# Performance work log

Measured on AMD Instinct MI355X. Metric: run time of the kernel, lower is better.

## Reference

```python
import jax, jax.numpy as jnp
import numpy as np

N = 100000   # nodes
F = 32       # input features
E = 1600000  # edges
G = 512      # graphs
EPS = 1e-5   # BatchNorm eps


def setup_inputs() -> dict:
    key = jax.random.key(0)
    ks = jax.random.split(key, 12)
    x = jax.random.normal(ks[0], (N, F), jnp.float32)
    edge_index = jax.random.randint(ks[1], (2, E), 0, N)
    batch = jnp.sort(jax.random.randint(ks[2], (N,), 0, G))

    def glorot(k, i, o):
        return jax.random.normal(k, (i, o), jnp.float32) * (1.0 / np.sqrt(i))

    return {
        "x": x, "edge_index": edge_index, "batch": batch,
        "W1": glorot(ks[3], F, 16), "b1": jnp.zeros((16,), jnp.float32),
        "g1": jnp.ones((16,), jnp.float32), "be1": jnp.zeros((16,), jnp.float32),
        "W2": glorot(ks[4], 16, 64), "b2": jnp.zeros((64,), jnp.float32),
        "g2": jnp.ones((64,), jnp.float32), "be2": jnp.zeros((64,), jnp.float32),
        "W3": glorot(ks[5], 64, 64), "b3": jnp.zeros((64,), jnp.float32),
        "Wc": glorot(ks[6], 64, 1), "bc": jnp.zeros((1,), jnp.float32),
    }


def _gcn_conv(h, src, dst, dis, W, b, n):
    # PyG GCNConv: D^{-1/2}(A+I)D^{-1/2} X W + b (self-loops folded in analytically)
    hw = h @ W                                   # [N, out]
    msg = hw[src] * (dis[src] * dis[dst])[:, None]   # gather + normalize, [E, out]
    agg = jax.ops.segment_sum(msg, dst, num_segments=n)  # scatter-add
    agg = agg + hw * (dis * dis)[:, None]        # self-loop contribution
    return agg + b


def _bn(h, g, b):
    # BatchNorm1d, training mode (biased variance over node axis)
    m = jnp.mean(h, axis=0)
    v = jnp.mean((h - m) ** 2, axis=0)
    return (h - m) * jax.lax.rsqrt(v + EPS) * g + b


def reference(x, edge_index, batch, W1, b1, g1, be1, W2, b2, g2, be2, W3, b3, Wc, bc):
    n = x.shape[0]
    src, dst = edge_index[0], edge_index[1]
    # degree including self-loops (computed on target nodes, edge weight 1)
    deg = jax.ops.segment_sum(jnp.ones((src.shape[0],), x.dtype), dst, num_segments=n) + 1.0
    dis = jax.lax.rsqrt(deg)

    h = jnp.tanh(_gcn_conv(x, src, dst, dis, W1, b1, n))
    h = _bn(h, g1, be1)
    h = jnp.tanh(_gcn_conv(h, src, dst, dis, W2, b2, n))
    h = _bn(h, g2, be2)
    h = jnp.tanh(_gcn_conv(h, src, dst, dis, W3, b3, n))

    # global_mean_pool over graph ids
    sums = jax.ops.segment_sum(h, batch, num_segments=G)          # [G, 64]
    cnts = jax.ops.segment_sum(jnp.ones((n,), x.dtype), batch, num_segments=G)
    pooled = sums / jnp.maximum(cnts, 1.0)[:, None]

    return pooled @ Wc + bc   # [G, 1]
```

## Files before the change

kernel.cpp:

```cpp
#include <hip/hip_runtime.h>

#define EPSV 1e-5f
#define EB 512
#define NPB 256
#define NBUK_MAX 512

typedef __attribute__((ext_vector_type(8))) short bf16x8;
typedef __attribute__((ext_vector_type(4))) float f32x4;
typedef unsigned short ushort_t;

__device__ inline unsigned f2bf(float f){
  unsigned u = __float_as_uint(f);
  u += 0x7fffu + ((u>>16)&1u);
  return u>>16;
}
#define BF_LO(u) __uint_as_float((u)<<16)
#define BF_HI(u) __uint_as_float((u)&0xffff0000u)

__global__ __launch_bounds__(256) void k_csr_count(const int* __restrict__ dst, int E, int chunk,
                                                   int nbuk, int* __restrict__ cnt){
  __shared__ int hist[NBUK_MAX];
  int t = threadIdx.x, b = blockIdx.x;
  for(int k=t; k<nbuk; k+=256) hist[k]=0;
  __syncthreads();
  int lo = b*chunk, hi = lo+chunk < E ? lo+chunk : E;
  for(int i=lo+t; i<hi; i+=256) atomicAdd(&hist[dst[i]>>8], 1);
  __syncthreads();
  for(int k=t; k<nbuk; k+=256) cnt[(size_t)k*EB + b] = hist[k];
}

__global__ __launch_bounds__(1024) void k_scan_local(const int* __restrict__ v_in, int L,
                                                     int* __restrict__ loc, int* __restrict__ blk){
  __shared__ int ps[1024];
  int t = threadIdx.x;
  int i = blockIdx.x*1024 + t;
  int v = (i < L) ? v_in[i] : 0;
  ps[t] = v;
  __syncthreads();
  for(int off=1; off<1024; off<<=1){
    int u = (t>=off) ? ps[t-off] : 0;
    __syncthreads();
    ps[t] += u;
    __syncthreads();
  }
  if(i < L) loc[i] = ps[t] - v;
  if(t == 1023) blk[blockIdx.x] = ps[t];
}

__global__ __launch_bounds__(1024) void k_scan_sums(int* __restrict__ blk, int nb,
                                                    int* __restrict__ totalOut){
  __shared__ int ps[1024];
  int t = threadIdx.x;
  int v = (t < nb) ? blk[t] : 0;
  ps[t] = v;
  __syncthreads();
  for(int off=1; off<1024; off<<=1){
    int u = (t>=off) ? ps[t-off] : 0;
    __syncthreads();
    ps[t] += u;
    __syncthreads();
  }
  if(t < nb) blk[t] = ps[t] - v;
  if(t == 1023) *totalOut = ps[t];
}

__global__ __launch_bounds__(256) void k_csr_scatter(const int* __restrict__ src,
                                                     const int* __restrict__ dst,
                                                     const int* __restrict__ loc,
                                                     const int* __restrict__ blk,
                                                     int E, int chunk, int nbuk,
                                                     unsigned* __restrict__ epk){
  __shared__ int cur[NBUK_MAX];
  int t = threadIdx.x, b = blockIdx.x;
  for(int k=t; k<nbuk; k+=256){
    int i = k*EB + b;
    cur[k] = loc[i] + blk[i>>10];
  }
  __syncthreads();
  int lo = b*chunk, hi = lo+chunk < E ? lo+chunk : E;
  for(int i=lo+t; i<hi; i+=256){
    int d = dst[i];
    int p = atomicAdd(&cur[d>>8], 1);
    epk[p] = ((unsigned)src[i]<<8) | (unsigned)(d & 255);
  }
}

__global__ __launch_bounds__(256) void k_csr_final(const unsigned* __restrict__ epk,
                                                   const int* __restrict__ loc,
                                                   const int* __restrict__ blk,
                                                   int nbuk, int N, int E,
                                                   int* __restrict__ rp, float* __restrict__ dis,
                                                   int* __restrict__ csr_src){
  __shared__ int hist[NPB], ps[NPB], cur[NPB];
  int t = threadIdx.x, k = blockIdx.x;
  int i0 = k*EB;
  int base = loc[i0] + blk[i0>>10];
  int next;
  if(k+1 < nbuk){ int i1 = (k+1)*EB; next = loc[i1] + blk[i1>>10]; }
  else next = E;
  int cntk = next - base;
  int node0 = k*NPB;
  hist[t] = 0;
  __syncthreads();
  for(int i=t; i<cntk; i+=256) atomicAdd(&hist[(int)(epk[base+i] & 255u)], 1);
  __syncthreads();
  int deg = hist[t];
  ps[t] = deg;
  __syncthreads();
  for(int off=1; off<256; off<<=1){
    int u = (t>=off) ? ps[t-off] : 0;
    __syncthreads();
    ps[t] += u;
    __syncthreads();
  }
  int lb = ps[t] - deg;
  int n = node0 + t;
  if(n < N){
    rp[n]  = base + lb;
    dis[n] = rsqrtf((float)deg + 1.0f);
  }
  cur[t] = base + lb;
  __syncthreads();
  for(int i=t; i<cntk; i+=256){
    unsigned e = epk[base+i];
    int p = atomicAdd(&cur[(int)(e & 255u)], 1);
    csr_src[p] = (int)(e >> 8);
  }
  if(k == nbuk-1 && t == 0) rp[N] = E;
}

__global__ __launch_bounds__(256) void k_gemm1(const float* __restrict__ x,
                                               const float* __restrict__ W,
                                               const float* __restrict__ dis,
                                               int N, ushort_t* __restrict__ P1){
  __shared__ __align__(16) float Ws[32*16];
  int t = threadIdx.x;
  for(int i=t; i<32*16; i+=256) Ws[i] = W[i];
  __syncthreads();
  int row = blockIdx.x*256 + t;
  if(row >= N) return;
  const float4* xr = (const float4*)(x + (size_t)row*32);
  float acc[16];
  #pragma unroll
  for(int j=0;j<16;j++) acc[j]=0.f;
  #pragma unroll
  for(int k4=0;k4<8;k4++){
    float4 v = xr[k4];
    float vv[4] = {v.x, v.y, v.z, v.w};
    #pragma unroll
    for(int kk=0;kk<4;kk++){
      float h = vv[kk];
      const float* wr = &Ws[(k4*4+kk)*16];
      #pragma unroll
      for(int j=0;j<16;j++) acc[j] += h*wr[j];
    }
  }
  float d = dis[row];
  unsigned q[8];
  #pragma unroll
  for(int j=0;j<8;j++)
    q[j] = f2bf(acc[2*j]*d) | (f2bf(acc[2*j+1]*d)<<16);
  uint4* o = (uint4*)(P1 + (size_t)row*16);
  o[0] = make_uint4(q[0],q[1],q[2],q[3]);
  o[1] = make_uint4(q[4],q[5],q[6],q[7]);
}

__global__ __launch_bounds__(256) void k_gather1(const int* __restrict__ rp,
    const int* __restrict__ csr_src,
    const float* __restrict__ dis, const ushort_t* __restrict__ P1,
    const float* __restrict__ bias, int N, ushort_t* __restrict__ Q1,
    float* __restrict__ sdis, float* __restrict__ partials){
  int t = threadIdx.x;
  int idx = blockIdx.x*256 + t;
  int n = idx >> 1, g = t & 1;
  float v[8];
  #pragma unroll
  for(int j=0;j<8;j++) v[j]=0.f;

  if(n < N){
    int beg = rp[n], end = rp[n+1];
    uint4 u = *(const uint4*)(P1 + (size_t)n*16 + g*8);
    float a0 = BF_LO(u.x), a1 = BF_HI(u.x), a2 = BF_LO(u.y), a3 = BF_HI(u.y);
    float a4 = BF_LO(u.z), a5 = BF_HI(u.z), a6 = BF_LO(u.w), a7 = BF_HI(u.w);
    float b0=0.f,b1=0.f,b2=0.f,b3=0.f,b4=0.f,b5=0.f,b6=0.f,b7=0.f;
    float sd = 0.f;
    int j = beg;
    for(; j+1 < end; j += 2){
      int s0 = csr_src[j], s1 = csr_src[j+1];
      uint4 u0 = *(const uint4*)(P1 + (size_t)s0*16 + g*8);
      uint4 u1 = *(const uint4*)(P1 + (size_t)s1*16 + g*8);
      if(g==0) sd += dis[s0] + dis[s1];
      a0 += BF_LO(u0.x); a1 += BF_HI(u0.x); a2 += BF_LO(u0.y); a3 += BF_HI(u0.y);
      a4 += BF_LO(u0.z); a5 += BF_HI(u0.z); a6 += BF_LO(u0.w); a7 += BF_HI(u0.w);
      b0 += BF_LO(u1.x); b1 += BF_HI(u1.x); b2 += BF_LO(u1.y); b3 += BF_HI(u1.y);
      b4 += BF_LO(u1.z); b5 += BF_HI(u1.z); b6 += BF_LO(u1.w); b7 += BF_HI(u1.w);
    }
    if(j < end){
      int s0 = csr_src[j];
      uint4 u0 = *(const uint4*)(P1 + (size_t)s0*16 + g*8);
      if(g==0) sd += dis[s0];
      a0 += BF_LO(u0.x); a1 += BF_HI(u0.x); a2 += BF_LO(u0.y); a3 += BF_HI(u0.y);
      a4 += BF_LO(u0.z); a5 += BF_HI(u0.z); a6 += BF_LO(u0.w); a7 += BF_HI(u0.w);
    }
    float d = dis[n];
    float4 bb0 = *(const float4*)(bias + g*8);
    float4 bb1 = *(const float4*)(bias + g*8 + 4);
    v[0] = tanhf((a0+b0)*d + bb0.x); v[1] = tanhf((a1+b1)*d + bb0.y);
    v[2] = tanhf((a2+b2)*d + bb0.z); v[3] = tanhf((a3+b3)*d + bb0.w);
    v[4] = tanhf((a4+b4)*d + bb1.x); v[5] = tanhf((a5+b5)*d + bb1.y);
    v[6] = tanhf((a6+b6)*d + bb1.z); v[7] = tanhf((a7+b7)*d + bb1.w);
    uint4 o;
    o.x = f2bf(v[0]*d) | (f2bf(v[1]*d)<<16);
    o.y = f2bf(v[2]*d) | (f2bf(v[3]*d)<<16);
    o.z = f2bf(v[4]*d) | (f2bf(v[5]*d)<<16);
    o.w = f2bf(v[6]*d) | (f2bf(v[7]*d)<<16);
    *(uint4*)(Q1 + (size_t)n*16 + g*8) = o;
    if(g==0) sdis[n] = sd;
  }

  int lane = t & 63, wid = t >> 6;
  __shared__ float redS[4][2][8], redQ[4][2][8];
  #pragma unroll
  for(int j=0;j<8;j++){
    float s = v[j], q = v[j]*v[j];
    #pragma unroll
    for(int off=32; off>=2; off>>=1){
      s += __shfl_down(s, off, 64);
      q += __shfl_down(q, off, 64);
    }
    if(lane < 2){ redS[wid][lane][j] = s; redQ[wid][lane][j] = q; }
  }
  __syncthreads();
  if(t < 16){
    int gg = t>>3, j = t&7;
    float S = redS[0][gg][j]+redS[1][gg][j]+redS[2][gg][j]+redS[3][gg][j];
    float Q = redQ[0][gg][j]+redQ[1][gg][j]+redQ[2][gg][j]+redQ[3][gg][j];
    partials[(size_t)blockIdx.x*32 + t]      = S;
    partials[(size_t)blockIdx.x*32 + 16 + t] = Q;
  }
}

template<int C>
__global__ __launch_bounds__(256) void k_bn_red(const float* __restrict__ partials, int nblk,
                                                float* __restrict__ red){
  constexpr int W = 2*C;
  constexpr int RPF = 256/W;
  int t = threadIdx.x;
  int c = t % W, r0 = t / W;
  float acc = 0.f;
  for(int r = blockIdx.x*RPF + r0; r < nblk; r += 64*RPF)
    acc += partials[(size_t)r*W + c];
  __shared__ float ls[256];
  ls[t] = acc;
  __syncthreads();
  if(t < W){
    float s = 0.f;
    #pragma unroll
    for(int k=0;k<RPF;k++) s += ls[k*W + t];
    red[blockIdx.x*W + t] = s;
  }
}

template<int C>
__global__ __launch_bounds__(256) void k_bn_finprep2(const float* __restrict__ red,
                           const float* __restrict__ gw, const float* __restrict__ be,
                           float invN, const float* __restrict__ W,
                           float* __restrict__ Wp, float* __restrict__ cp){
  __shared__ float s0[C], s1[C], scf[C], shf[C];
  int t = threadIdx.x;
  if(t < 2*C){
    float s = 0.f;
    for(int r=0;r<64;r++) s += red[r*2*C + t];
    if(t < C) s0[t] = s; else s1[t-C] = s;
  }
  __syncthreads();
  if(t < C){
    float m = s0[t]*invN;
    float var = fmaxf(s1[t]*invN - m*m, 0.f);
    float inv = rsqrtf(var + EPSV);
    float sc = gw[t]*inv;
    scf[t] = sc;
    shf[t] = be[t] - m*sc;
  }
  __syncthreads();
  for(int i=t; i<C*64; i+=256){
    int k = i >> 6;
    Wp[i] = scf[k]*W[i];
  }
  if(t < 64){
    float s = 0.f;
    for(int k=0;k<C;k++) s += shf[k]*W[k*64 + t];
    cp[t] = s;
  }
}

__global__ __launch_bounds__(256) void k_bn_finprep3(const float* __restrict__ red,
                           const float* __restrict__ gw, const float* __restrict__ be,
                           float invN, const float* __restrict__ W,
                           ushort_t* __restrict__ wf, float* __restrict__ cp){
  __shared__ float s0[64], s1[64], scf[64], shf[64];
  int t = threadIdx.x;
  if(t < 128){
    float s = 0.f;
    for(int r=0;r<64;r++) s += red[r*128 + t];
    if(t < 64) s0[t] = s; else s1[t-64] = s;
  }
  __syncthreads();
  if(t < 64){
    float m = s0[t]*invN;
    float var = fmaxf(s1[t]*invN - m*m, 0.f);
    float inv = rsqrtf(var + EPSV);
    float sc = gw[t]*inv;
    scf[t] = sc;
    shf[t] = be[t] - m*sc;
  }
  __syncthreads();
  int total = 4*2*64*8;
  for(int idx=t; idx<total; idx+=256){
    int e = idx & 7;
    int l = (idx>>3) & 63;
    int slot = idx>>9;
    int ct = slot>>1, half = slot&1;
    int k = (l>>4)*8 + e + half*32;
    int col = ct*16 + (l&15);
    wf[idx] = (ushort_t)f2bf(scf[k]*W[k*64 + col]);
  }
  if(t < 64){
    float s = 0.f;
    for(int k=0;k<64;k++) s += shf[k]*W[k*64 + t];
    cp[t] = s;
  }
}

__global__ __launch_bounds__(256) void k_l2fused(const int* __restrict__ rp,
    const int* __restrict__ csr_src, const float* __restrict__ dis,
    const float* __restrict__ sdis, const ushort_t* __restrict__ Q1,
    const float* __restrict__ Wp, const float* __restrict__ cp,
    const float* __restrict__ bias, int N, ushort_t* __restrict__ Q2,
    float* __restrict__ partials){
  __shared__ __align__(16) float Wl[16*64];
  __shared__ float cpl[64], bl[64];
  int t = threadIdx.x;
  for(int i=t; i<16*64; i+=256) Wl[i] = Wp[i];
  if(t < 64){ cpl[t] = cp[t]; bl[t] = bias[t]; }
  __syncthreads();

  int idx = blockIdx.x*256 + t;
  int n = idx >> 3, g = t & 7;
  int half = g & 1, eo = g >> 1;
  bool valid = (n < N);
  float M8[8];
  #pragma unroll
  for(int j=0;j<8;j++) M8[j]=0.f;

  if(valid){
    int beg = rp[n], end = rp[n+1];
    if(eo == 0){
      uint4 u = *(const uint4*)(Q1 + (size_t)n*16 + half*8);
      M8[0]+=BF_LO(u.x); M8[1]+=BF_HI(u.x); M8[2]+=BF_LO(u.y); M8[3]+=BF_HI(u.y);
      M8[4]+=BF_LO(u.z); M8[5]+=BF_HI(u.z); M8[6]+=BF_LO(u.w); M8[7]+=BF_HI(u.w);
    }
    for(int j=beg+eo; j<end; j+=4){
      int s = csr_src[j];
      uint4 u = *(const uint4*)(Q1 + (size_t)s*16 + half*8);
      M8[0]+=BF_LO(u.x); M8[1]+=BF_HI(u.x); M8[2]+=BF_LO(u.y); M8[3]+=BF_HI(u.y);
      M8[4]+=BF_LO(u.z); M8[5]+=BF_HI(u.z); M8[6]+=BF_LO(u.w); M8[7]+=BF_HI(u.w);
    }
  }
  #pragma unroll
  for(int j=0;j<8;j++){
    float m = M8[j];
    m += __shfl_xor(m, 2, 64);
    m += __shfl_xor(m, 4, 64);
    M8[j] = m;
  }
  float M16[16];
  #pragma unroll
  for(int j=0;j<8;j++){
    float o = __shfl_xor(M8[j], 1, 64);
    M16[j]   = (half==0) ? M8[j] : o;
    M16[8+j] = (half==0) ? o     : M8[j];
  }

  float v[8];
  #pragma unroll
  for(int j=0;j<8;j++) v[j]=0.f;
  if(valid){
    float d = dis[n];
    float sg = sdis[n] + d;
    int c0 = g*8;
    float acc[8];
    #pragma unroll
    for(int j=0;j<8;j++) acc[j] = cpl[c0+j]*sg;
    #pragma unroll
    for(int k=0;k<16;k++){
      float m = M16[k];
      float4 w0 = *(const float4*)&Wl[k*64 + c0];
      float4 w1 = *(const float4*)&Wl[k*64 + c0 + 4];
      acc[0]+=m*w0.x; acc[1]+=m*w0.y; acc[2]+=m*w0.z; acc[3]+=m*w0.w;
      acc[4]+=m*w1.x; acc[5]+=m*w1.y; acc[6]+=m*w1.z; acc[7]+=m*w1.w;
    }
    #pragma unroll
    for(int j=0;j<8;j++) v[j] = tanhf(d*acc[j] + bl[c0+j]);
    uint4 o;
    o.x = f2bf(v[0]*d) | (f2bf(v[1]*d)<<16);
    o.y = f2bf(v[2]*d) | (f2bf(v[3]*d)<<16);
    o.z = f2bf(v[4]*d) | (f2bf(v[5]*d)<<16);
    o.w = f2bf(v[6]*d) | (f2bf(v[7]*d)<<16);
    *(uint4*)(Q2 + (size_t)n*64 + c0) = o;
  }

  int lane = t & 63, wid = t >> 6;
  __shared__ float redS[4][8][8], redQ[4][8][8];
  #pragma unroll
  for(int j=0;j<8;j++){
    float s = v[j], q = v[j]*v[j];
    #pragma unroll
    for(int off=32; off>=8; off>>=1){
      s += __shfl_down(s, off, 64);
      q += __shfl_down(q, off, 64);
    }
    if(lane < 8){ redS[wid][lane][j] = s; redQ[wid][lane][j] = q; }
  }
  __syncthreads();
  if(t < 64){
    int gg = t>>3, j = t&7;
    float S = redS[0][gg][j]+redS[1][gg][j]+redS[2][gg][j]+redS[3][gg][j];
    float Q = redQ[0][gg][j]+redQ[1][gg][j]+redQ[2][gg][j]+redQ[3][gg][j];
    partials[(size_t)blockIdx.x*128 + t]      = S;
    partials[(size_t)blockIdx.x*128 + 64 + t] = Q;
  }
}

__global__ __launch_bounds__(256) void k_gather3(const int* __restrict__ rp,
    const int* __restrict__ csr_src, const ushort_t* __restrict__ Q2,
    int N, ushort_t* __restrict__ M3){
  int t = threadIdx.x;
  int idx = blockIdx.x*256 + t;
  int n = idx >> 3, g = t & 7;
  if(n >= N) return;
  int beg = rp[n], end = rp[n+1];
  uint4 u = *(const uint4*)(Q2 + (size_t)n*64 + g*8);
  float a0 = BF_LO(u.x), a1 = BF_HI(u.x), a2 = BF_LO(u.y), a3 = BF_HI(u.y);
  float a4 = BF_LO(u.z), a5 = BF_HI(u.z), a6 = BF_LO(u.w), a7 = BF_HI(u.w);
  float b0=0.f,b1=0.f,b2=0.f,b3=0.f,b4=0.f,b5=0.f,b6=0.f,b7=0.f;
  int j = beg;
  for(; j+1 < end; j += 2){
    int s0 = csr_src[j], s1 = csr_src[j+1];
    uint4 u0 = *(const uint4*)(Q2 + (size_t)s0*64 + g*8);
    uint4 u1 = *(const uint4*)(Q2 + (size_t)s1*64 + g*8);
    a0 += BF_LO(u0.x); a1 += BF_HI(u0.x); a2 += BF_LO(u0.y); a3 += BF_HI(u0.y);
    a4 += BF_LO(u0.z); a5 += BF_HI(u0.z); a6 += BF_LO(u0.w); a7 += BF_HI(u0.w);
    b0 += BF_LO(u1.x); b1 += BF_HI(u1.x); b2 += BF_LO(u1.y); b3 += BF_HI(u1.y);
    b4 += BF_LO(u1.z); b5 += BF_HI(u1.z); b6 += BF_LO(u1.w); b7 += BF_HI(u1.w);
  }
  if(j < end){
    int s0 = csr_src[j];
    uint4 u0 = *(const uint4*)(Q2 + (size_t)s0*64 + g*8);
    a0 += BF_LO(u0.x); a1 += BF_HI(u0.x); a2 += BF_LO(u0.y); a3 += BF_HI(u0.y);
    a4 += BF_LO(u0.z); a5 += BF_HI(u0.z); a6 += BF_LO(u0.w); a7 += BF_HI(u0.w);
  }
  uint4 o;
  o.x = f2bf(a0+b0) | (f2bf(a1+b1)<<16);
  o.y = f2bf(a2+b2) | (f2bf(a3+b3)<<16);
  o.z = f2bf(a4+b4) | (f2bf(a5+b5)<<16);
  o.w = f2bf(a6+b6) | (f2bf(a7+b7)<<16);
  *(uint4*)(M3 + (size_t)n*64 + g*8) = o;
}

__global__ __launch_bounds__(256) void k_mfma_head(const ushort_t* __restrict__ M3,
                                                   const ushort_t* __restrict__ wf,
                                                   const float* __restrict__ cp,
                                                   const float* __restrict__ dis,
                                                   const float* __restrict__ sdis,
                                                   const float* __restrict__ b3,
                                                   const float* __restrict__ Wc,
                                                   int N, float* __restrict__ y){
  int t = threadIdx.x, wid = t>>6, l = t&63;
  int r0 = blockIdx.x*128 + wid*32;

  bf16x8 bfr[4][2];
  #pragma unroll
  for(int ct=0; ct<4; ct++)
    #pragma unroll
    for(int h=0; h<2; h++)
      bfr[ct][h] = *(const bf16x8*)(wf + ((size_t)(ct*2+h)*64 + l)*8);

  bf16x8 af[2][2];
  #pragma unroll
  for(int rt=0; rt<2; rt++){
    int arow = r0 + rt*16 + (l&15);
    int k0 = (l>>4)*8;
    #pragma unroll
    for(int h=0; h<2; h++){
      if(arow < N) af[rt][h] = *(const bf16x8*)(M3 + (size_t)arow*64 + k0 + h*32);
      else         af[rt][h] = (bf16x8){0,0,0,0,0,0,0,0};
    }
  }

  f32x4 acc[2][4];
  #pragma unroll
  for(int rt=0; rt<2; rt++)
    #pragma unroll
    for(int ct=0; ct<4; ct++)
      acc[rt][ct] = (f32x4){0.f,0.f,0.f,0.f};

  #pragma unroll
  for(int rt=0; rt<2; rt++)
    #pragma unroll
    for(int ct=0; ct<4; ct++)
      #pragma unroll
      for(int h=0; h<2; h++)
        acc[rt][ct] = __builtin_amdgcn_mfma_f32_16x16x32_bf16(af[rt][h], bfr[ct][h], acc[rt][ct], 0, 0, 0);

  float cpc[4], blc[4], wcc[4];
  #pragma unroll
  for(int ct=0; ct<4; ct++){
    int col = ct*16 + (l&15);
    cpc[ct] = cp[col]; blc[ct] = b3[col]; wcc[ct] = Wc[col];
  }

  #pragma unroll
  for(int rt=0; rt<2; rt++){
    int rbase = r0 + rt*16 + (l>>4)*4;
    #pragma unroll
    for(int reg=0; reg<4; reg++){
      int row = rbase + reg;
      bool ok = (row < N);
      float d  = ok ? dis[row] : 0.f;
      float sg = ok ? (sdis[row] + d) : 0.f;
      float s = 0.f;
      #pragma unroll
      for(int ct=0; ct<4; ct++){
        float h = tanhf(d*(acc[rt][ct][reg] + sg*cpc[ct]) + blc[ct]);
        s += h*wcc[ct];
      }
      s += __shfl_xor(s, 1, 64);
      s += __shfl_xor(s, 2, 64);
      s += __shfl_xor(s, 4, 64);
      s += __shfl_xor(s, 8, 64);
      if(ok && (l&15)==0) y[row] = s;
    }
  }
}

__global__ __launch_bounds__(64) void k_pool2(const float* __restrict__ y,
                                              const int* __restrict__ batch, int N,
                                              const float* __restrict__ bc,
                                              float* __restrict__ out){
  int gId = blockIdx.x;
  int t = threadIdx.x;
  int lo=0, hi=N;
  while(lo<hi){ int mid=(lo+hi)>>1; if(batch[mid] < gId) lo=mid+1; else hi=mid; }
  int start = lo;
  lo=start; hi=N;
  while(lo<hi){ int mid=(lo+hi)>>1; if(batch[mid] < gId+1) lo=mid+1; else hi=mid; }
  int end = lo;

  float s = 0.f;
  for(int r = start+t; r < end; r += 64) s += y[r];
  #pragma unroll
  for(int o=32; o>0; o>>=1) s += __shfl_down(s, o, 64);
  if(t == 0){
    float cnt = (float)(end - start);
    out[gId] = s / fmaxf(cnt, 1.0f) + bc[0];
  }
}

extern "C" void kernel_launch(void* const* d_in, const int* in_sizes, int n_in,
                              void* d_out, int out_size, void* d_ws, size_t ws_size,
                              hipStream_t stream) {
  const float* x     = (const float*)d_in[0];
  const int*   ei    = (const int*)d_in[1];
  const int*   batch = (const int*)d_in[2];
  const float* W1 = (const float*)d_in[3];
  const float* b1 = (const float*)d_in[4];
  const float* g1 = (const float*)d_in[5];
  const float* be1= (const float*)d_in[6];
  const float* W2 = (const float*)d_in[7];
  const float* b2 = (const float*)d_in[8];
  const float* g2 = (const float*)d_in[9];
  const float* be2= (const float*)d_in[10];
  const float* W3 = (const float*)d_in[11];
  const float* b3 = (const float*)d_in[12];
  const float* Wc = (const float*)d_in[13];
  const float* bc = (const float*)d_in[14];

  int N = in_sizes[2];
  int E = in_sizes[1] / 2;
  int G = out_size;
  const int* srcp = ei;
  const int* dstp = ei + E;
  float* out = (float*)d_out;

  auto cdiv = [](long long a, long long b){ return (int)((a+b-1)/b); };
  auto al16 = [](size_t s){ return (s + 15) & ~(size_t)15; };
  int nbuk  = cdiv(N, NPB);
  int chunk = cdiv(E, EB);
  int L     = nbuk * EB;
  int nbL   = cdiv(L, 1024);
  int nblk16 = cdiv((long long)N*2, 256);
  int nblk64 = cdiv((long long)N*8, 256);

  char* w = (char*)d_ws;
  ushort_t* Q1       = (ushort_t*)w; w += al16((size_t)N*16*2);
  ushort_t* P1       = (ushort_t*)w; w += al16((size_t)N*16*2);
  ushort_t* Q2       = (ushort_t*)w; w += al16((size_t)N*64*2);
  ushort_t* M3       = (ushort_t*)w; w += al16((size_t)N*64*2);
  float*    dis      = (float*)w;    w += al16((size_t)N*4);
  float*    sdis     = (float*)w;    w += al16((size_t)N*4);
  float*    yv       = (float*)w;    w += al16((size_t)N*4);
  int*      row_ptr  = (int*)w;      w += al16((size_t)(N+1)*4);
  int*      csr_src  = (int*)w;      w += al16((size_t)E*4);
  unsigned* epk      = (unsigned*)w; w += al16((size_t)E*4);
  int*      cnt      = (int*)w;      w += al16((size_t)L*4);
  int*      scan_loc = (int*)w;      w += al16((size_t)L*4);
  int*      scan_blk = (int*)w;      w += al16(1024*4);
  float*    partials = (float*)w;    w += al16((size_t)nblk64*128*4);
  float*    red      = (float*)w;    w += al16(64*128*4);
  float*    Wp       = (float*)w;    w += al16(16*64*4);
  float*    cp       = (float*)w;    w += al16(64*4);
  ushort_t* wf       = (ushort_t*)w; w += al16(8*64*8*2);

  k_csr_count<<<EB,256,0,stream>>>(dstp, E, chunk, nbuk, cnt);
  k_scan_local<<<nbL,1024,0,stream>>>(cnt, L, scan_loc, scan_blk);
  k_scan_sums<<<1,1024,0,stream>>>(scan_blk, nbL, row_ptr + N);
  k_csr_scatter<<<EB,256,0,stream>>>(srcp, dstp, scan_loc, scan_blk, E, chunk, nbuk, epk);
  k_csr_final<<<nbuk,256,0,stream>>>(epk, scan_loc, scan_blk, nbuk, N, E, row_ptr, dis, csr_src);

  k_gemm1<<<cdiv(N,256),256,0,stream>>>(x, W1, dis, N, P1);
  k_gather1<<<nblk16,256,0,stream>>>(row_ptr, csr_src, dis, P1, b1, N, Q1, sdis, partials);
  k_bn_red<16><<<64,256,0,stream>>>(partials, nblk16, red);
  k_bn_finprep2<16><<<1,256,0,stream>>>(red, g1, be1, 1.0f/N, W2, Wp, cp);

  k_l2fused<<<nblk64,256,0,stream>>>(row_ptr, csr_src, dis, sdis, Q1, Wp, cp, b2, N, Q2, partials);
  k_bn_red<64><<<64,256,0,stream>>>(partials, nblk64, red);
  k_bn_finprep3<<<1,256,0,stream>>>(red, g2, be2, 1.0f/N, W3, wf, cp);

  k_gather3<<<nblk64,256,0,stream>>>(row_ptr, csr_src, Q2, N, M3);
  k_mfma_head<<<cdiv(N,128),256,0,stream>>>(M3, wf, cp, dis, sdis, b3, Wc, N, yv);

  k_pool2<<<G,64,0,stream>>>(yv, batch, N, bc, out);
}
```

Baseline: 202.0 us.

## Split layer-2 fused kernel into a gather kernel and an MFMA transform kernel

Replaces the fused layer-2 kernel, which gathered with 8 threads per node and did a scalar 16x64 matmul, with two kernels. A lean gather uses 2 threads per node with unrolled neighbour loads and writes the aggregated 16-wide features as bf16. An MFMA kernel then applies the BN-folded W2 (packed to bf16 fragments, zero-padded to K=32) with tanh and BN statistics. This lowers thread redundancy in the gather and moves the matmul onto matrix cores, at the cost of an extra launch, an N×16 intermediate round-trip, and strided 2-byte output stores.

```diff
diff --git a/kernel.cpp b/kernel.cpp
--- a/kernel.cpp
+++ b/kernel.cpp
@@ -261,20 +261,19 @@
   }
 }
 
-template<int C>
-__global__ __launch_bounds__(256) void k_bn_finprep2(const float* __restrict__ red,
+__global__ __launch_bounds__(256) void k_bn_finprep2b(const float* __restrict__ red,
                            const float* __restrict__ gw, const float* __restrict__ be,
                            float invN, const float* __restrict__ W,
-                           float* __restrict__ Wp, float* __restrict__ cp){
-  __shared__ float s0[C], s1[C], scf[C], shf[C];
-  int t = threadIdx.x;
-  if(t < 2*C){
+                           ushort_t* __restrict__ wf, float* __restrict__ cp){
+  __shared__ float s0[16], s1[16], scf[16], shf[16];
+  int t = threadIdx.x;
+  if(t < 32){
     float s = 0.f;
-    for(int r=0;r<64;r++) s += red[r*2*C + t];
-    if(t < C) s0[t] = s; else s1[t-C] = s;
-  }
-  __syncthreads();
-  if(t < C){
+    for(int r=0;r<64;r++) s += red[r*32 + t];
+    if(t < 16) s0[t] = s; else s1[t-16] = s;
+  }
+  __syncthreads();
+  if(t < 16){
     float m = s0[t]*invN;
     float var = fmaxf(s1[t]*invN - m*m, 0.f);
     float inv = rsqrtf(var + EPSV);
@@ -283,13 +282,19 @@
     shf[t] = be[t] - m*sc;
   }
   __syncthreads();
-  for(int i=t; i<C*64; i+=256){
-    int k = i >> 6;
-    Wp[i] = scf[k]*W[i];
+  int total = 4*64*8;
+  for(int idx=t; idx<total; idx+=256){
+    int e = idx & 7;
+    int l = (idx>>3) & 63;
+    int ct = idx>>9;
+    int k = (l>>4)*8 + e;
+    int col = ct*16 + (l&15);
+    float v = (k < 16) ? scf[k]*W[k*64 + col] : 0.f;
+    wf[idx] = (ushort_t)f2bf(v);
   }
   if(t < 64){
     float s = 0.f;
-    for(int k=0;k<C;k++) s += shf[k]*W[k*64 + t];
+    for(int k=0;k<16;k++) s += shf[k]*W[k*64 + t];
     cp[t] = s;
   }
 }
@@ -332,101 +337,125 @@
   }
 }
 
-__global__ __launch_bounds__(256) void k_l2fused(const int* __restrict__ rp,
-    const int* __restrict__ csr_src, const float* __restrict__ dis,
-    const float* __restrict__ sdis, const ushort_t* __restrict__ Q1,
-    const float* __restrict__ Wp, const float* __restrict__ cp,
-    const float* __restrict__ bias, int N, ushort_t* __restrict__ Q2,
-    float* __restrict__ partials){
-  __shared__ __align__(16) float Wl[16*64];
-  __shared__ float cpl[64], bl[64];
-  int t = threadIdx.x;
-  for(int i=t; i<16*64; i+=256) Wl[i] = Wp[i];
-  if(t < 64){ cpl[t] = cp[t]; bl[t] = bias[t]; }
-  __syncthreads();
-
+__global__ __launch_bounds__(256) void k_gather2(const int* __restrict__ rp,
+    const int* __restrict__ csr_src, const ushort_t* __restrict__ Q1,
+    int N, ushort_t* __restrict__ M2){
+  int t = threadIdx.x;
   int idx = blockIdx.x*256 + t;
-  int n = idx >> 3, g = t & 7;
-  int half = g & 1, eo = g >> 1;
-  bool valid = (n < N);
-  float M8[8];
-  #pragma unroll
-  for(int j=0;j<8;j++) M8[j]=0.f;
-
-  if(valid){
-    int beg = rp[n], end = rp[n+1];
-    if(eo == 0){
-      uint4 u = *(const uint4*)(Q1 + (size_t)n*16 + half*8);
-      M8[0]+=BF_LO(u.x); M8[1]+=BF_HI(u.x); M8[2]+=BF_LO(u.y); M8[3]+=BF_HI(u.y);
-      M8[4]+=BF_LO(u.z); M8[5]+=BF_HI(u.z); M8[6]+=BF_LO(u.w); M8[7]+=BF_HI(u.w);
-    }
-    for(int j=beg+eo; j<end; j+=4){
-      int s = csr_src[j];
-      uint4 u = *(const uint4*)(Q1 + (size_t)s*16 + half*8);
-      M8[0]+=BF_LO(u.x); M8[1]+=BF_HI(u.x); M8[2]+=BF_LO(u.y); M8[3]+=BF_HI(u.y);
-      M8[4]+=BF_LO(u.z); M8[5]+=BF_HI(u.z); M8[6]+=BF_LO(u.w); M8[7]+=BF_HI(u.w);
-    }
-  }
-  #pragma unroll
-  for(int j=0;j<8;j++){
-    float m = M8[j];
-    m += __shfl_xor(m, 2, 64);
-    m += __shfl_xor(m, 4, 64);
-    M8[j] = m;
-  }
-  float M16[16];
-  #pragma unroll
-  for(int j=0;j<8;j++){
-    float o = __shfl_xor(M8[j], 1, 64);
-    M16[j]   = (half==0) ? M8[j] : o;
-    M16[8+j] = (half==0) ? o     : M8[j];
-  }
-
-  float v[8];
-  #pragma unroll
-  for(int j=0;j<8;j++) v[j]=0.f;
-  if(valid){
-    float d = dis[n];
-    float sg = sdis[n] + d;
-    int c0 = g*8;
-    float acc[8];
-    #pragma unroll
-    for(int j=0;j<8;j++) acc[j] = cpl[c0+j]*sg;
-    #pragma unroll
-    for(int k=0;k<16;k++){
-      float m = M16[k];
-      float4 w0 = *(const float4*)&Wl[k*64 + c0];
-      float4 w1 = *(const float4*)&Wl[k*64 + c0 + 4];
-      acc[0]+=m*w0.x; acc[1]+=m*w0.y; acc[2]+=m*w0.z; acc[3]+=m*w0.w;
-      acc[4]+=m*w1.x; acc[5]+=m*w1.y; acc[6]+=m*w1.z; acc[7]+=m*w1.w;
-    }
-    #pragma unroll
-    for(int j=0;j<8;j++) v[j] = tanhf(d*acc[j] + bl[c0+j]);
-    uint4 o;
-    o.x = f2bf(v[0]*d) | (f2bf(v[1]*d)<<16);
-    o.y = f2bf(v[2]*d) | (f2bf(v[3]*d)<<16);
-    o.z = f2bf(v[4]*d) | (f2bf(v[5]*d)<<16);
-    o.w = f2bf(v[6]*d) | (f2bf(v[7]*d)<<16);
-    *(uint4*)(Q2 + (size_t)n*64 + c0) = o;
-  }
-
-  int lane = t & 63, wid = t >> 6;
-  __shared__ float redS[4][8][8], redQ[4][8][8];
-  #pragma unroll
-  for(int j=0;j<8;j++){
-    float s = v[j], q = v[j]*v[j];
-    #pragma unroll
-    for(int off=32; off>=8; off>>=1){
-      s += __shfl_down(s, off, 64);
-      q += __shfl_down(q, off, 64);
-    }
-    if(lane < 8){ redS[wid][lane][j] = s; redQ[wid][lane][j] = q; }
+  int n = idx >> 1, g = t & 1;
+  if(n >= N) return;
+  int beg = rp[n], end = rp[n+1];
+  uint4 u = *(const uint4*)(Q1 + (size_t)n*16 + g*8);
+  float a0 = BF_LO(u.x), a1 = BF_HI(u.x), a2 = BF_LO(u.y), a3 = BF_HI(u.y);
+  float a4 = BF_LO(u.z), a5 = BF_HI(u.z), a6 = BF_LO(u.w), a7 = BF_HI(u.w);
+  float b0=0.f,b1=0.f,b2=0.f,b3=0.f,b4=0.f,b5=0.f,b6=0.f,b7=0.f;
+  int j = beg;
+  for(; j+1 < end; j += 2){
+    int s0 = csr_src[j], s1 = csr_src[j+1];
+    uint4 u0 = *(const uint4*)(Q1 + (size_t)s0*16 + g*8);
+    uint4 u1 = *(const uint4*)(Q1 + (size_t)s1*16 + g*8);
+    a0 += BF_LO(u0.x); a1 += BF_HI(u0.x); a2 += BF_LO(u0.y); a3 += BF_HI(u0.y);
+    a4 += BF_LO(u0.z); a5 += BF_HI(u0.z); a6 += BF_LO(u0.w); a7 += BF_HI(u0.w);
+    b0 += BF_LO(u1.x); b1 += BF_HI(u1.x); b2 += BF_LO(u1.y); b3 += BF_HI(u1.y);
+    b4 += BF_LO(u1.z); b5 += BF_HI(u1.z); b6 += BF_LO(u1.w); b7 += BF_HI(u1.w);
+  }
+  if(j < end){
+    int s0 = csr_src[j];
+    uint4 u0 = *(const uint4*)(Q1 + (size_t)s0*16 + g*8);
+    a0 += BF_LO(u0.x); a1 += BF_HI(u0.x); a2 += BF_LO(u0.y); a3 += BF_HI(u0.y);
+    a4 += BF_LO(u0.z); a5 += BF_HI(u0.z); a6 += BF_LO(u0.w); a7 += BF_HI(u0.w);
+  }
+  uint4 o;
+  o.x = f2bf(a0+b0) | (f2bf(a1+b1)<<16);
+  o.y = f2bf(a2+b2) | (f2bf(a3+b3)<<16);
+  o.z = f2bf(a4+b4) | (f2bf(a5+b5)<<16);
+  o.w = f2bf(a6+b6) | (f2bf(a7+b7)<<16);
+  *(uint4*)(M2 + (size_t)n*16 + g*8) = o;
+}
+
+__global__ __launch_bounds__(256) void k_mfma2(const ushort_t* __restrict__ M2,
+                                               const ushort_t* __restrict__ wf,
+                                               const float* __restrict__ cp,
+                                               const float* __restrict__ dis,
+                                               const float* __restrict__ sdis,
+                                               const float* __restrict__ b2,
+                                               int N, ushort_t* __restrict__ Q2,
+                                               float* __restrict__ partials){
+  int t = threadIdx.x, wid = t>>6, l = t&63;
+  int r0 = blockIdx.x*128 + wid*32;
+
+  bf16x8 bfr[4];
+  #pragma unroll
+  for(int ct=0; ct<4; ct++)
+    bfr[ct] = *(const bf16x8*)(wf + ((size_t)ct*64 + l)*8);
+
+  bf16x8 af[2];
+  #pragma unroll
+  for(int rt=0; rt<2; rt++){
+    int arow = r0 + rt*16 + (l&15);
+    int k0 = (l>>4)*8;
+    if(arow < N && k0 < 16) af[rt] = *(const bf16x8*)(M2 + (size_t)arow*16 + k0);
+    else                    af[rt] = (bf16x8){0,0,0,0,0,0,0,0};
+  }
+
+  f32x4 acc[2][4];
+  #pragma unroll
+  for(int rt=0; rt<2; rt++)
+    #pragma unroll
+    for(int ct=0; ct<4; ct++)
+      acc[rt][ct] = (f32x4){0.f,0.f,0.f,0.f};
+
+  #pragma unroll
+  for(int rt=0; rt<2; rt++)
+    #pragma unroll
+    for(int ct=0; ct<4; ct++)
+      acc[rt][ct] = __builtin_amdgcn_mfma_f32_16x16x32_bf16(af[rt], bfr[ct], acc[rt][ct], 0, 0, 0);
+
+  float cpc[4], blc[4];
+  #pragma unroll
+  for(int ct=0; ct<4; ct++){
+    int col = ct*16 + (l&15);
+    cpc[ct] = cp[col]; blc[ct] = b2[col];
+  }
+
+  float S4[4] = {0.f,0.f,0.f,0.f}, Q4[4] = {0.f,0.f,0.f,0.f};
+  #pragma unroll
+  for(int rt=0; rt<2; rt++){
+    int rbase = r0 + rt*16 + (l>>4)*4;
+    #pragma unroll
+    for(int reg=0; reg<4; reg++){
+      int row = rbase + reg;
+      if(row < N){
+        float d = dis[row];
+        float sg = sdis[row] + d;
+        #pragma unroll
+        for(int ct=0; ct<4; ct++){
+          float h = tanhf(d*(acc[rt][ct][reg] + sg*cpc[ct]) + blc[ct]);
+          Q2[(size_t)row*64 + ct*16 + (l&15)] = (ushort_t)f2bf(h*d);
+          S4[ct] += h; Q4[ct] += h*h;
+        }
+      }
+    }
+  }
+  #pragma unroll
+  for(int ct=0; ct<4; ct++){
+    S4[ct] += __shfl_xor(S4[ct], 16, 64);
+    S4[ct] += __shfl_xor(S4[ct], 32, 64);
+    Q4[ct] += __shfl_xor(Q4[ct], 16, 64);
+    Q4[ct] += __shfl_xor(Q4[ct], 32, 64);
+  }
+  __shared__ float wsm[4][64], wqm[4][64];
+  if(l < 16){
+    #pragma unroll
+    for(int ct=0; ct<4; ct++){
+      wsm[wid][ct*16 + l] = S4[ct];
+      wqm[wid][ct*16 + l] = Q4[ct];
+    }
   }
   __syncthreads();
   if(t < 64){
-    int gg = t>>3, j = t&7;
-    float S = redS[0][gg][j]+redS[1][gg][j]+redS[2][gg][j]+redS[3][gg][j];
-    float Q = redQ[0][gg][j]+redQ[1][gg][j]+redQ[2][gg][j]+redQ[3][gg][j];
+    float S = wsm[0][t]+wsm[1][t]+wsm[2][t]+wsm[3][t];
+    float Q = wqm[0][t]+wqm[1][t]+wqm[2][t]+wqm[3][t];
     partials[(size_t)blockIdx.x*128 + t]      = S;
     partials[(size_t)blockIdx.x*128 + 64 + t] = Q;
   }
@@ -601,10 +630,12 @@
   int nbL   = cdiv(L, 1024);
   int nblk16 = cdiv((long long)N*2, 256);
   int nblk64 = cdiv((long long)N*8, 256);
+  int nblkM  = cdiv(N, 128);
 
   char* w = (char*)d_ws;
   ushort_t* Q1       = (ushort_t*)w; w += al16((size_t)N*16*2);
   ushort_t* P1       = (ushort_t*)w; w += al16((size_t)N*16*2);
+  ushort_t* M2       = (ushort_t*)w; w += al16((size_t)N*16*2);
   ushort_t* Q2       = (ushort_t*)w; w += al16((size_t)N*64*2);
   ushort_t* M3       = (ushort_t*)w; w += al16((size_t)N*64*2);
   float*    dis      = (float*)w;    w += al16((size_t)N*4);
@@ -618,7 +649,6 @@
   int*      scan_blk = (int*)w;      w += al16(1024*4);
   float*    partials = (float*)w;    w += al16((size_t)nblk64*128*4);
   float*    red      = (float*)w;    w += al16(64*128*4);
-  float*    Wp       = (float*)w;    w += al16(16*64*4);
   float*    cp       = (float*)w;    w += al16(64*4);
   ushort_t* wf       = (ushort_t*)w; w += al16(8*64*8*2);
 
@@ -631,10 +661,11 @@
   k_gemm1<<<cdiv(N,256),256,0,stream>>>(x, W1, dis, N, P1);
   k_gather1<<<nblk16,256,0,stream>>>(row_ptr, csr_src, dis, P1, b1, N, Q1, sdis, partials);
   k_bn_red<16><<<64,256,0,stream>>>(partials, nblk16, red);
-  k_bn_finprep2<16><<<1,256,0,stream>>>(red, g1, be1, 1.0f/N, W2, Wp, cp);
-
-  k_l2fused<<<nblk64,256,0,stream>>>(row_ptr, csr_src, dis, sdis, Q1, Wp, cp, b2, N, Q2, partials);
-  k_bn_red<64><<<64,256,0,stream>>>(partials, nblk64, red);
+  k_bn_finprep2b<<<1,256,0,stream>>>(red, g1, be1, 1.0f/N, W2, wf, cp);
+
+  k_gather2<<<nblk16,256,0,stream>>>(row_ptr, csr_src, Q1, N, M2);
+  k_mfma2<<<nblkM,256,0,stream>>>(M2, wf, cp, dis, sdis, b2, N, Q2, partials);
+  k_bn_red<64><<<64,256,0,stream>>>(partials, nblkM, red);
   k_bn_finprep3<<<1,256,0,stream>>>(red, g2, be2, 1.0f/N, W3, wf, cp);
 
   k_gather3<<<nblk64,256,0,stream>>>(row_ptr, csr_src, Q2, N, M3);
```

After: 187.2 us. 7.3% less time.
